# Performance work log

Measured on AMD Instinct MI355X. Metric: run time of the kernel, lower is better.

## Reference

```python
import jax, jax.numpy as jnp
import numpy as np

N = 25000      # nodes
E = 400000     # edges
IN = 1024      # in_channels
FC = 128       # feature_channels
ADD = 20       # additional_channels
MID = (FC + ADD) // 4   # 37, fc1 output (heads=4)
OUT = 3
EPS = 1e-5
NEG_SLOPE = 0.01


def setup_inputs() -> dict:
    key = jax.random.key(0)
    ks = jax.random.split(key, 16)
    d = {}
    d["features"] = jax.random.normal(ks[0], (N, IN), dtype=jnp.float32)
    d["edges"] = jax.random.randint(ks[1], (2, E), 0, N, dtype=jnp.int64)
    d["edges2"] = jax.random.randint(ks[2], (2, 1000), 0, N, dtype=jnp.int64)
    d["edge_features"] = jax.random.normal(ks[3], (E, 1), dtype=jnp.float32)
    d["additional_feature"] = jax.random.normal(ks[4], (N, ADD), dtype=jnp.float32)
    # SAGEConv params: lin_l (neighbor path, with bias), lin_r (root path, no bias)
    s = 1.0 / np.sqrt(IN)
    d["Wl"] = jax.random.uniform(ks[5], (FC, IN), jnp.float32, -s, s)
    d["bl"] = jax.random.uniform(ks[6], (FC,), jnp.float32, -s, s)
    d["Wr"] = jax.random.uniform(ks[7], (FC, IN), jnp.float32, -s, s)
    s1 = 1.0 / np.sqrt(FC + ADD)
    d["W1"] = jax.random.uniform(ks[8], (MID, FC + ADD), jnp.float32, -s1, s1)
    d["b1"] = jax.random.uniform(ks[9], (MID,), jnp.float32, -s1, s1)
    s2 = 1.0 / np.sqrt(MID)
    d["W2"] = jax.random.uniform(ks[10], (OUT, MID), jnp.float32, -s2, s2)
    d["b2"] = jax.random.uniform(ks[11], (OUT,), jnp.float32, -s2, s2)
    # BatchNorm1d (eval mode -> running stats)
    d["gamma"] = jnp.ones((MID,), jnp.float32)
    d["beta"] = jnp.zeros((MID,), jnp.float32)
    d["run_mean"] = jax.random.normal(ks[12], (MID,), dtype=jnp.float32) * 0.1
    d["run_var"] = jnp.abs(jax.random.normal(ks[13], (MID,), dtype=jnp.float32)) * 0.1 + 1.0
    return d


def reference(features, edges, edges2, edge_features, additional_feature,
              Wl, bl, Wr, W1, b1, W2, b2, gamma, beta, run_mean, run_var):
    src, dst = edges[0], edges[1]  # PyG: messages flow source -> target
    # scatter-mean of neighbor features onto targets
    agg = jax.ops.segment_sum(features[src], dst, num_segments=N)        # [N, IN]
    deg = jax.ops.segment_sum(jnp.ones((E,), features.dtype), dst, num_segments=N)
    agg = agg / jnp.maximum(deg, 1.0)[:, None]
    # SAGEConv: lin_l(mean_neigh) + lin_r(x)
    x = agg @ Wl.T + bl + features @ Wr.T                                 # [N, FC]
    x = jnp.where(x >= 0, x, NEG_SLOPE * x)                               # leaky_relu
    # dropout is identity in eval mode
    x = jnp.concatenate([x, additional_feature], axis=1) @ W1.T + b1      # [N, MID]
    x = jnp.maximum(x, 0.0)                                               # relu
    x = gamma * (x - run_mean) * jax.lax.rsqrt(run_var + EPS) + beta      # BN eval
    return x @ W2.T + b2                                                  # [N, OUT]
```

## Files before the change

### kernel.cpp

```cpp
#include <hip/hip_runtime.h>

#define N_NODES 25000
#define N_EDGES 400000
#define IN_CH 1024
#define FC 128
#define ADD_CH 20
#define XCH 148
#define MID 37
#define OUT_CH 3
#define MAXDEG 64

typedef short bf16x8 __attribute__((ext_vector_type(8)));
typedef float f32x4 __attribute__((ext_vector_type(4)));

__device__ __forceinline__ unsigned int f2bf(float x) {
    unsigned int u = __builtin_bit_cast(unsigned int, x);
    unsigned int lsb = (u >> 16) & 1u;
    u += 0x7fffu + lsb;
    return u >> 16;
}
__device__ __forceinline__ unsigned int pkbf(float a, float b) {
    return f2bf(a) | (f2bf(b) << 16);
}
__device__ __forceinline__ float bflo(unsigned int v) {
    return __builtin_bit_cast(float, v << 16);
}
__device__ __forceinline__ float bfhi(unsigned int v) {
    return __builtin_bit_cast(float, v & 0xffff0000u);
}

#define WSWZ_B 16
#define BUILD_B 782

__global__ __launch_bounds__(512) void prep_build(const float* __restrict__ Wl,
                                                  const float* __restrict__ Wr,
                                                  ushort* __restrict__ Wpk,
                                                  const int* __restrict__ edges,
                                                  int* __restrict__ cursor,
                                                  int* __restrict__ col) {
    int b = blockIdx.x, t = threadIdx.x;
    if (b < WSWZ_B) {
        int w = t >> 6, lane = t & 63, l15 = lane & 15, q8 = (lane >> 4) * 8;
        int ch = b * 16 + l15;
        const float* src = (ch < FC) ? (Wl + (size_t)ch * IN_CH)
                                     : (Wr + (size_t)(ch - FC) * IN_CH);
        #pragma unroll
        for (int j = 0; j < 4; ++j) {
            int kt = w * 4 + j;
            float4 lo = *(const float4*)(src + kt * 32 + q8);
            float4 hi = *(const float4*)(src + kt * 32 + q8 + 4);
            uint4 pk;
            pk.x = pkbf(lo.x, lo.y); pk.y = pkbf(lo.z, lo.w);
            pk.z = pkbf(hi.x, hi.y); pk.w = pkbf(hi.z, hi.w);
            ((uint4*)Wpk)[(size_t)(b * 32 + kt) * 64 + lane] = pk;
        }
    } else {
        int e = (b - WSWZ_B) * 512 + t;
        if (e < N_EDGES) {
            int dst = edges[N_EDGES + e];
            int pos = atomicAdd(&cursor[dst], 1);
            if (pos < MAXDEG) col[dst * MAXDEG + pos] = edges[e];
        }
    }
}

#define GEMM_B 782

__global__ __launch_bounds__(512, 4) void gemm(const float* __restrict__ A,
                                               const ushort* __restrict__ Wpk,
                                               ushort* __restrict__ Py,
                                               ushort* __restrict__ Pz) {
    __shared__ __align__(16) ushort Fs[2 * 32 * 64 * 8];
    int b = blockIdx.x, t = threadIdx.x;
    int w = t >> 6, lane = t & 63;
    int l15 = lane & 15, q = lane >> 4;
    int m0 = b * 32;

    const bf16x8* W0 = (const bf16x8*)Wpk + (size_t)(w * 2 + 0) * 32 * 64 + lane;
    const bf16x8* W1 = (const bf16x8*)Wpk + (size_t)(w * 2 + 1) * 32 * 64 + lane;
    bf16x8 aw[2][2], an[2][2], bw[2][2], bn[2][2];
    aw[0][0] = W0[0];  aw[0][1] = W1[0];
    aw[1][0] = W0[64]; aw[1][1] = W1[64];

    {
        int r = t >> 4;
        int p0 = t & 15;
        int row = m0 + r; if (row >= N_NODES) row = N_NODES - 1;
        const float* src = A + (size_t)row * IN_CH;
        int g = r >> 4, l = r & 15;
        #pragma unroll
        for (int h = 0; h < 2; ++h) {
            float4 lo[4], hi[4];
            #pragma unroll
            for (int m = 0; m < 4; ++m) {
                int o = (h * 4 + m) * 16 + p0;
                lo[m] = *(const float4*)(src + o * 8);
                hi[m] = *(const float4*)(src + o * 8 + 4);
            }
            #pragma unroll
            for (int m = 0; m < 4; ++m) {
                int o = (h * 4 + m) * 16 + p0;
                int kt = o >> 2, qq = o & 3;
                uint4 pk;
                pk.x = pkbf(lo[m].x, lo[m].y); pk.y = pkbf(lo[m].z, lo[m].w);
                pk.z = pkbf(hi[m].x, hi[m].y); pk.w = pkbf(hi[m].z, hi[m].w);
                int u = (g * 32 + kt) * 64 + qq * 16 + ((l + qq) & 15);
                *(uint4*)&Fs[(size_t)u * 8] = pk;
            }
        }
    }
    __syncthreads();

    int ru = q * 16 + ((l15 + q) & 15);
    const bf16x8* F0 = (const bf16x8*)Fs + ru;
    const bf16x8* F1 = (const bf16x8*)Fs + 32 * 64 + ru;

    f32x4 acc[2][2] = {};
    bw[0][0] = F0[0];  bw[0][1] = F1[0];
    bw[1][0] = F0[64]; bw[1][1] = F1[64];

    #pragma unroll
    for (int kt = 0; kt < 32; kt += 2) {
        int kn = kt + 2;
        if (kn < 32) {
            an[0][0] = W0[(size_t)kn * 64];       an[0][1] = W1[(size_t)kn * 64];
            an[1][0] = W0[(size_t)(kn + 1) * 64]; an[1][1] = W1[(size_t)(kn + 1) * 64];
            bn[0][0] = F0[(size_t)kn * 64];       bn[0][1] = F1[(size_t)kn * 64];
            bn[1][0] = F0[(size_t)(kn + 1) * 64]; bn[1][1] = F1[(size_t)(kn + 1) * 64];
        }
        #pragma unroll
        for (int j = 0; j < 2; ++j)
            #pragma unroll
            for (int cf = 0; cf < 2; ++cf) {
                acc[cf][0] = __builtin_amdgcn_mfma_f32_16x16x32_bf16(aw[j][cf], bw[j][0], acc[cf][0], 0, 0, 0);
                acc[cf][1] = __builtin_amdgcn_mfma_f32_16x16x32_bf16(aw[j][cf], bw[j][1], acc[cf][1], 0, 0, 0);
            }
        if (kn < 32) {
            #pragma unroll
            for (int j = 0; j < 2; ++j)
                #pragma unroll
                for (int cf = 0; cf < 2; ++cf) {
                    aw[j][cf] = an[j][cf];
                    bw[j][cf] = bn[j][cf];
                }
        }
    }
    #pragma unroll
    for (int g = 0; g < 2; ++g) {
        int node = m0 + g * 16 + l15;
        if (node < N_NODES) {
            ushort* base = (w < 4) ? (Py + (size_t)node * FC + w * 32)
                                   : (Pz + (size_t)node * FC + (w - 4) * 32);
            #pragma unroll
            for (int cf = 0; cf < 2; ++cf) {
                f32x4 v = acc[cf][g];
                uint2 pk;
                pk.x = pkbf(v[0], v[1]);
                pk.y = pkbf(v[2], v[3]);
                *(uint2*)(base + cf * 16 + q * 4) = pk;
            }
        }
    }
}

__global__ __launch_bounds__(256) void fused_tail(const ushort* __restrict__ Py,
                                                  const ushort* __restrict__ Pz,
                                                  const int* __restrict__ deg,
                                                  const int* __restrict__ col,
                                                  const float* __restrict__ addf,
                                                  const float* __restrict__ bl,
                                                  const float* __restrict__ W1,
                                                  const float* __restrict__ b1,
                                                  const float* __restrict__ W2,
                                                  const float* __restrict__ b2,
                                                  const float* __restrict__ gamma,
                                                  const float* __restrict__ beta,
                                                  const float* __restrict__ rmean,
                                                  const float* __restrict__ rvar,
                                                  float* __restrict__ out) {
    __shared__ float W1s[XCH][MID + 3];
    __shared__ float xbuf[4][XCH + 4];
    __shared__ float hbuf[4][MID + 3];
    int t = threadIdx.x;
    for (int idx = t; idx < MID * XCH; idx += 256) {
        int j = idx / XCH, k = idx - j * XCH;
        W1s[k][j] = W1[idx];
    }
    __syncthreads();
    int w = t >> 6, lane = t & 63;
    int n = blockIdx.x * 4 + w;
    bool valid = (n < N_NODES);
    int d = valid ? deg[n] : 0;
    if (d > MAXDEG) d = MAXDEG;
    int g = lane >> 4, c16 = lane & 15;
    float s[8] = {0.f, 0.f, 0.f, 0.f, 0.f, 0.f, 0.f, 0.f};
    if (d > 0) {
        int cidx = col[n * MAXDEG + (lane < d ? lane : 0)];
        for (int i = 0; i < d; i += 16) {
            int e[4];
            uint4 v[4];
            #pragma unroll
            for (int j = 0; j < 4; ++j) {
                int ee = i + g + j * 4;
                e[j] = __shfl(cidx, (ee < d) ? ee : 0);
            }
            #pragma unroll
            for (int j = 0; j < 4; ++j)
                v[j] = *(const uint4*)&Py[(size_t)e[j] * FC + c16 * 8];
            #pragma unroll
            for (int j = 0; j < 4; ++j) {
                if (i + g + j * 4 < d) {
                    s[0] += bflo(v[j].x); s[1] += bfhi(v[j].x);
                    s[2] += bflo(v[j].y); s[3] += bfhi(v[j].y);
                    s[4] += bflo(v[j].z); s[5] += bfhi(v[j].z);
                    s[6] += bflo(v[j].w); s[7] += bfhi(v[j].w);
                }
            }
        }
        #pragma unroll
        for (int r = 0; r < 8; ++r) {
            s[r] += __shfl_xor(s[r], 16);
            s[r] += __shfl_xor(s[r], 32);
        }
    }
    if (valid) {
        if (lane < 16) {
            #pragma unroll
            for (int r = 0; r < 8; ++r) xbuf[w][lane * 8 + r] = s[r];
        }
        float invd = 1.0f / (float)(d > 1 ? d : 1);
        unsigned int vr = *(const unsigned int*)&Pz[(size_t)n * FC + lane * 2];
        float x0 = xbuf[w][2 * lane] * invd + bl[2 * lane] + bflo(vr);
        float x1 = xbuf[w][2 * lane + 1] * invd + bl[2 * lane + 1] + bfhi(vr);
        x0 = (x0 >= 0.f) ? x0 : 0.01f * x0;
        x1 = (x1 >= 0.f) ? x1 : 0.01f * x1;
        xbuf[w][2 * lane] = x0;
        xbuf[w][2 * lane + 1] = x1;
        if (lane < ADD_CH) xbuf[w][FC + lane] = addf[(size_t)n * ADD_CH + lane];
        if (lane < MID) {
            float h = b1[lane];
            #pragma unroll 4
            for (int k = 0; k < XCH; ++k) h += W1s[k][lane] * xbuf[w][k];
            h = fmaxf(h, 0.0f);
            h = gamma[lane] * (h - rmean[lane]) * rsqrtf(rvar[lane] + 1e-5f) + beta[lane];
            hbuf[w][lane] = h;
        }
        if (lane < OUT_CH) {
            float o = b2[lane];
            #pragma unroll
            for (int j = 0; j < MID; ++j) o += W2[lane * MID + j] * hbuf[w][j];
            out[(size_t)n * OUT_CH + lane] = o;
        }
    }
}


extern "C" void kernel_launch(void* const* d_in, const int* in_sizes, int n_in,
                              void* d_out, int out_size, void* d_ws, size_t ws_size,
                              hipStream_t stream) {
    const float* features = (const float*)d_in[0];
    const int*   edges    = (const int*)d_in[1];
    const float* addf     = (const float*)d_in[4];
    const float* Wl       = (const float*)d_in[5];
    const float* bl       = (const float*)d_in[6];
    const float* Wr       = (const float*)d_in[7];
    const float* W1       = (const float*)d_in[8];
    const float* b1       = (const float*)d_in[9];
    const float* W2       = (const float*)d_in[10];
    const float* b2       = (const float*)d_in[11];
    const float* gamma    = (const float*)d_in[12];
    const float* beta     = (const float*)d_in[13];
    const float* rmean    = (const float*)d_in[14];
    const float* rvar     = (const float*)d_in[15];
    float* out = (float*)d_out;

    char* ws = (char*)d_ws;
    size_t off = 0;
    ushort* Py = (ushort*)(ws + off);     off += (size_t)N_NODES * FC * 2;
    ushort* Pz = (ushort*)(ws + off);     off += (size_t)N_NODES * FC * 2;
    ushort* Wpk = (ushort*)(ws + off);    off += (size_t)16 * 32 * 64 * 16;
    int* cursor = (int*)(ws + off);       off += (size_t)N_NODES * 4;
    int* col = (int*)(ws + off);          off += (size_t)N_NODES * MAXDEG * 4;

    hipMemsetAsync(cursor, 0, (size_t)N_NODES * 4, stream);

    prep_build<<<WSWZ_B + BUILD_B, 512, 0, stream>>>(Wl, Wr, Wpk, edges, cursor, col);

    gemm<<<GEMM_B, 512, 0, stream>>>(features, Wpk, Py, Pz);

    fused_tail<<<(N_NODES + 3) / 4, 256, 0, stream>>>(Py, Pz, cursor, col, addf, bl,
                                                      W1, b1, W2, b2, gamma, beta,
                                                      rmean, rvar, out);
}
```

Baseline: 284.4 us.

## Restructure GEMM into double-buffered async global-to-LDS K-loop with 64-row tiles

```diff
diff --git a/kernel.cpp b/kernel.cpp
--- a/kernel.cpp
+++ b/kernel.cpp
@@ -27,6 +27,13 @@
 }
 __device__ __forceinline__ float bfhi(unsigned int v) {
     return __builtin_bit_cast(float, v & 0xffff0000u);
+}
+
+__device__ __forceinline__ void gload16(const void* g, void* l) {
+    __builtin_amdgcn_global_load_lds(
+        (const __attribute__((address_space(1))) unsigned int*)g,
+        (__attribute__((address_space(3))) unsigned int*)l,
+        16, 0, 0);
 }
 
 #define WSWZ_B 16
@@ -52,7 +59,7 @@
             uint4 pk;
             pk.x = pkbf(lo.x, lo.y); pk.y = pkbf(lo.z, lo.w);
             pk.z = pkbf(hi.x, hi.y); pk.w = pkbf(hi.z, hi.w);
-            ((uint4*)Wpk)[(size_t)(b * 32 + kt) * 64 + lane] = pk;
+            ((uint4*)Wpk)[((size_t)kt * 16 + b) * 64 + lane] = pk;
         }
     } else {
         int e = (b - WSWZ_B) * 512 + t;
@@ -64,100 +71,81 @@
     }
 }
 
-#define GEMM_B 782
-
-__global__ __launch_bounds__(512, 4) void gemm(const float* __restrict__ A,
+#define GEMM_B 391
+
+__global__ __launch_bounds__(512, 6) void gemm(const float* __restrict__ A,
                                                const ushort* __restrict__ Wpk,
                                                ushort* __restrict__ Py,
                                                ushort* __restrict__ Pz) {
-    __shared__ __align__(16) ushort Fs[2 * 32 * 64 * 8];
-    int b = blockIdx.x, t = threadIdx.x;
+    __shared__ uint4 LDS[2][1536];
+    int t = threadIdx.x;
+    int b = blockIdx.x;
+    int m0 = b * 64;
+
+    int ga = t >> 7, hq = (t >> 6) & 1, la = t & 63;
+    int nodeA = m0 + ga * 16 + (la & 15);
+    if (nodeA >= N_NODES) nodeA = N_NODES - 1;
+    const float* Asrc = A + (size_t)nodeA * IN_CH + (la >> 4) * 8 + hq * 4;
+    const uint4* Wg = (const uint4*)Wpk;
+    int tb = t & ~63;
+
     int w = t >> 6, lane = t & 63;
+    int wm = w >> 2, wn = w & 3;
     int l15 = lane & 15, q = lane >> 4;
-    int m0 = b * 32;
-
-    const bf16x8* W0 = (const bf16x8*)Wpk + (size_t)(w * 2 + 0) * 32 * 64 + lane;
-    const bf16x8* W1 = (const bf16x8*)Wpk + (size_t)(w * 2 + 1) * 32 * 64 + lane;
-    bf16x8 aw[2][2], an[2][2], bw[2][2], bn[2][2];
-    aw[0][0] = W0[0];  aw[0][1] = W1[0];
-    aw[1][0] = W0[64]; aw[1][1] = W1[64];
+
+    f32x4 acc[4][2] = {};
 
     {
-        int r = t >> 4;
-        int p0 = t & 15;
-        int row = m0 + r; if (row >= N_NODES) row = N_NODES - 1;
-        const float* src = A + (size_t)row * IN_CH;
-        int g = r >> 4, l = r & 15;
-        #pragma unroll
-        for (int h = 0; h < 2; ++h) {
-            float4 lo[4], hi[4];
-            #pragma unroll
-            for (int m = 0; m < 4; ++m) {
-                int o = (h * 4 + m) * 16 + p0;
-                lo[m] = *(const float4*)(src + o * 8);
-                hi[m] = *(const float4*)(src + o * 8 + 4);
-            }
-            #pragma unroll
-            for (int m = 0; m < 4; ++m) {
-                int o = (h * 4 + m) * 16 + p0;
-                int kt = o >> 2, qq = o & 3;
-                uint4 pk;
-                pk.x = pkbf(lo[m].x, lo[m].y); pk.y = pkbf(lo[m].z, lo[m].w);
-                pk.z = pkbf(hi[m].x, hi[m].y); pk.w = pkbf(hi[m].z, hi[m].w);
-                int u = (g * 32 + kt) * 64 + qq * 16 + ((l + qq) & 15);
-                *(uint4*)&Fs[(size_t)u * 8] = pk;
-            }
-        }
+        const uint4* ws = Wg;
+        gload16(ws + t,        &LDS[0][tb]);
+        gload16(ws + 512 + t,  &LDS[0][512 + tb]);
+        gload16(Asrc,          &LDS[0][1024 + tb]);
     }
     __syncthreads();
 
-    int ru = q * 16 + ((l15 + q) & 15);
-    const bf16x8* F0 = (const bf16x8*)Fs + ru;
-    const bf16x8* F1 = (const bf16x8*)Fs + 32 * 64 + ru;
-
-    f32x4 acc[2][2] = {};
-    bw[0][0] = F0[0];  bw[0][1] = F1[0];
-    bw[1][0] = F0[64]; bw[1][1] = F1[64];
+    for (int c = 0; c < 32; ++c) {
+        int cur = c & 1;
+        if (c + 1 < 32) {
+            const uint4* ws = Wg + (size_t)(c + 1) * 1024;
+            gload16(ws + t,       &LDS[cur ^ 1][tb]);
+            gload16(ws + 512 + t, &LDS[cur ^ 1][512 + tb]);
+            gload16(Asrc + (size_t)(c + 1) * 32, &LDS[cur ^ 1][1024 + tb]);
+        }
+        bf16x8 wf[4];
+        #pragma unroll
+        for (int i = 0; i < 4; ++i)
+            wf[i] = *(const bf16x8*)&LDS[cur][(wn * 4 + i) * 64 + lane];
+        bf16x8 af[2];
+        #pragma unroll
+        for (int g2 = 0; g2 < 2; ++g2) {
+            f32x4 lo = *(const f32x4*)&LDS[cur][1024 + ((wm * 2 + g2) * 2 + 0) * 64 + lane];
+            f32x4 hi = *(const f32x4*)&LDS[cur][1024 + ((wm * 2 + g2) * 2 + 1) * 64 + lane];
+            uint4 pk;
+            pk.x = pkbf(lo[0], lo[1]); pk.y = pkbf(lo[2], lo[3]);
+            pk.z = pkbf(hi[0], hi[1]); pk.w = pkbf(hi[2], hi[3]);
+            af[g2] = __builtin_bit_cast(bf16x8, pk);
+        }
+        #pragma unroll
+        for (int i = 0; i < 4; ++i)
+            #pragma unroll
+            for (int g2 = 0; g2 < 2; ++g2)
+                acc[i][g2] = __builtin_amdgcn_mfma_f32_16x16x32_bf16(wf[i], af[g2], acc[i][g2], 0, 0, 0);
+        __syncthreads();
+    }
 
     #pragma unroll
-    for (int kt = 0; kt < 32; kt += 2) {
-        int kn = kt + 2;
-        if (kn < 32) {
-            an[0][0] = W0[(size_t)kn * 64];       an[0][1] = W1[(size_t)kn * 64];
-            an[1][0] = W0[(size_t)(kn + 1) * 64]; an[1][1] = W1[(size_t)(kn + 1) * 64];
-            bn[0][0] = F0[(size_t)kn * 64];       bn[0][1] = F1[(size_t)kn * 64];
-            bn[1][0] = F0[(size_t)(kn + 1) * 64]; bn[1][1] = F1[(size_t)(kn + 1) * 64];
-        }
-        #pragma unroll
-        for (int j = 0; j < 2; ++j)
-            #pragma unroll
-            for (int cf = 0; cf < 2; ++cf) {
-                acc[cf][0] = __builtin_amdgcn_mfma_f32_16x16x32_bf16(aw[j][cf], bw[j][0], acc[cf][0], 0, 0, 0);
-                acc[cf][1] = __builtin_amdgcn_mfma_f32_16x16x32_bf16(aw[j][cf], bw[j][1], acc[cf][1], 0, 0, 0);
-            }
-        if (kn < 32) {
-            #pragma unroll
-            for (int j = 0; j < 2; ++j)
-                #pragma unroll
-                for (int cf = 0; cf < 2; ++cf) {
-                    aw[j][cf] = an[j][cf];
-                    bw[j][cf] = bn[j][cf];
-                }
-        }
-    }
-    #pragma unroll
-    for (int g = 0; g < 2; ++g) {
-        int node = m0 + g * 16 + l15;
+    for (int g2 = 0; g2 < 2; ++g2) {
+        int node = m0 + wm * 32 + g2 * 16 + l15;
         if (node < N_NODES) {
-            ushort* base = (w < 4) ? (Py + (size_t)node * FC + w * 32)
-                                   : (Pz + (size_t)node * FC + (w - 4) * 32);
-            #pragma unroll
-            for (int cf = 0; cf < 2; ++cf) {
-                f32x4 v = acc[cf][g];
+            ushort* base = (wn < 2) ? (Py + (size_t)node * FC + (wn & 1) * 64 + q * 4)
+                                    : (Pz + (size_t)node * FC + (wn & 1) * 64 + q * 4);
+            #pragma unroll
+            for (int i = 0; i < 4; ++i) {
+                f32x4 v = acc[i][g2];
                 uint2 pk;
                 pk.x = pkbf(v[0], v[1]);
                 pk.y = pkbf(v[2], v[3]);
-                *(uint2*)(base + cf * 16 + q * 4) = pk;
+                *(uint2*)(base + i * 16) = pk;
             }
         }
     }
@@ -278,7 +266,7 @@
     size_t off = 0;
     ushort* Py = (ushort*)(ws + off);     off += (size_t)N_NODES * FC * 2;
     ushort* Pz = (ushort*)(ws + off);     off += (size_t)N_NODES * FC * 2;
-    ushort* Wpk = (ushort*)(ws + off);    off += (size_t)16 * 32 * 64 * 16;
+    ushort* Wpk = (ushort*)(ws + off);    off += (size_t)32 * 16 * 64 * 16;
     int* cursor = (int*)(ws + off);       off += (size_t)N_NODES * 4;
     int* col = (int*)(ws + off);          off += (size_t)N_NODES * MAXDEG * 4;
 
```

Measured after the change: 273.5 us. 3.9% less time.
